# Kernel optimization log

Hardware: AMD Instinct MI355X
Metric: run time of the kernel (lower is better)

The kernel has to match this reference:

```python
import jax, jax.numpy as jnp
import numpy as np

# Model dims (match init_kwargs)
B, S, D = 4, 2048, 1024          # batch, seq, d_model
H, E, DH = 8, 4, 128             # n_heads, n_experts_attn, d_head
K = 2                            # k_attn (routed, n_expert_shared_attn=0)
NEG_INF = jnp.float32(-1e30)


def setup_inputs() -> dict:
    key = jax.random.key(0)
    ks = jax.random.split(key, 9)
    s = np.float32(1.0 / np.sqrt(D))
    return {
        "q_src": jax.random.normal(ks[0], (B, S, D), jnp.float32),
        "k_src": jax.random.normal(ks[1], (B, S, D), jnp.float32),
        "v_src": jax.random.normal(ks[2], (B, S, D), jnp.float32),
        "wq": jax.random.normal(ks[3], (H * DH, D), jnp.float32) * s,
        "wk": jax.random.normal(ks[4], (H * DH, D), jnp.float32) * s,
        "sel_v_w": jax.random.normal(ks[5], (H * E, D), jnp.float32) * s,
        "sel_o_w": jax.random.normal(ks[6], (H * E, D), jnp.float32) * s,
        "v_w": jax.random.normal(ks[7], (H, E, D, DH), jnp.float32) * s,
        "o_w": jax.random.normal(ks[8], (H, E, DH, D), jnp.float32) * np.float32(1.0 / np.sqrt(H * DH)),
        "bias_v": jnp.zeros((E,), jnp.float32),   # load-balancing bias buffer (zeros at init)
        "bias_o": jnp.zeros((E,), jnp.float32),
        # causal boolean mask, True = attend (skip_mask all True -> trimming is identity)
        "attn_mask": jnp.broadcast_to(jnp.tril(jnp.ones((S, S), bool)), (B, S, S)),
        "position_ids": jnp.broadcast_to(jnp.arange(S, dtype=jnp.int32), (B, S)),
        "skip_mask": jnp.ones((B, S), bool),
    }


def _expert_gate(x, w, bias):
    """Sigmoid gating + per-head top-k routed expert selection.
    Returns dense combine weights [b,s,h,E] (sum of sel_val * one_hot) and indices [b,s,h,K]."""
    logits = (x @ w.T).reshape(*x.shape[:-1], H, E)        # [b,s,h,E]
    sel = jax.nn.sigmoid(logits)
    # bias only affects *which* experts are picked (added under no_grad in torch)
    _, idx = jax.lax.top_k(jax.lax.stop_gradient(sel) + bias, K)  # [b,s,h,K]
    sel_val = jnp.take_along_axis(sel, idx, axis=-1)        # [b,s,h,K]
    gate = jnp.sum(jax.nn.one_hot(idx, E, dtype=sel.dtype) * sel_val[..., None], axis=-2)
    return gate, idx


def reference(q_src, k_src, v_src, wq, wk, sel_v_w, sel_o_w, v_w, o_w,
              bias_v, bias_o, attn_mask, position_ids, skip_mask):
    # scale.sqrt() applied to both q and k -> full 1/sqrt(d_head) on scores
    ssq = jnp.float32((1.0 / np.sqrt(DH)) ** 0.5)
    q = ((q_src @ wq.T) * ssq).reshape(B, S, H, DH).transpose(0, 2, 1, 3)  # [b,h,s,dh]
    k = ((k_src @ wk.T) * ssq).reshape(B, S, H, DH).transpose(0, 2, 1, 3)

    v_gate, v_idx = _expert_gate(k_src, sel_v_w, bias_v)    # V experts routed on k_src
    o_gate, o_idx = _expert_gate(q_src, sel_o_w, bias_o)    # O experts routed on q_src

    # expert-mixed V projection (cvmm): all experts then dense combine
    all_v = jnp.einsum('bsm,hemd->bshed', v_src, v_w)       # [b,s,h,E,dh]
    v = jnp.einsum('bshed,bshe->bhsd', all_v, v_gate)       # [b,h,s,dh]

    scores = jnp.einsum('bhqd,bhkd->bhqk', q, k)
    scores = jnp.where(attn_mask[:, None], scores, NEG_INF)
    attn = jax.nn.softmax(scores, axis=-1)
    out = jnp.einsum('bhqk,bhkd->bqhd', attn, v)            # [b,s,h,dh]

    # expert-mixed O projection, summed over heads
    scaled = out[..., None, :] * o_gate[..., None]          # [b,s,h,E,dh]
    res = jnp.einsum('bshed,hedm->bsm', scaled, o_w)        # [b,s,d_model]
    return res, (v_idx, o_idx)
```

## Files before the change

### kernel.cpp

```cpp
#include <hip/hip_runtime.h>
#include <cstdint>
#include <cstddef>

typedef __bf16 bf16;
typedef __bf16 bf16x4 __attribute__((ext_vector_type(4)));
typedef __bf16 bf16x8 __attribute__((ext_vector_type(8)));
typedef float  fx4    __attribute__((ext_vector_type(4)));


__device__ __forceinline__ void async16(const void* g, void* l) {
  __builtin_amdgcn_global_load_lds((const __attribute__((address_space(1))) void*)g,
                                   (__attribute__((address_space(3))) void*)l, 16, 0, 0);
}

#define BARRIER() do { asm volatile("" ::: "memory"); __builtin_amdgcn_s_barrier(); \
                       asm volatile("" ::: "memory"); } while (0)

template <int CTRL>
__device__ __forceinline__ float dppf(float x) {
  return __int_as_float(__builtin_amdgcn_update_dpp(
      0, __float_as_int(x), CTRL, 0xf, 0xf, true));
}

__global__ __launch_bounds__(256) void f32_to_bf16(const float4* __restrict__ src,
                                                   bf16x4* __restrict__ dst, int n4) {
  int i = blockIdx.x * 256 + threadIdx.x;
  if (i < n4) {
    float4 v = src[i];
    bf16x4 o;
    o[0] = (bf16)v.x; o[1] = (bf16)v.y; o[2] = (bf16)v.z; o[3] = (bf16)v.w;
    dst[i] = o;
  }
}

__global__ __launch_bounds__(256) void make_wvt(const float* __restrict__ v_w,
                                                bf16* __restrict__ wvt) {
  __shared__ float tile[64][65];
  const int he = blockIdx.z, k0 = blockIdx.x * 64, dh0 = blockIdx.y * 64;
  const float* in = v_w + (size_t)he * 1024 * 128;
  #pragma unroll
  for (int j = 0; j < 16; j++) {
    int idx = threadIdx.x + j * 256;
    int r = idx >> 6, c = idx & 63;
    tile[r][c] = in[(size_t)(k0 + r) * 128 + dh0 + c];
  }
  __syncthreads();
  const int h = he >> 2, e = he & 3;
  bf16* outp = wvt + ((size_t)(h * 128 + dh0) * 4 + e) * 1024 + k0;
  #pragma unroll
  for (int j = 0; j < 16; j++) {
    int idx = threadIdx.x + j * 256;
    int r = idx >> 6, c = idx & 63;
    outp[(size_t)r * 4096 + c] = (bf16)tile[c][r];
  }
}

__global__ __launch_bounds__(256) void make_wot(const float* __restrict__ o_w,
                                                bf16* __restrict__ wot) {
  __shared__ float tile[64][65];
  const int he = blockIdx.z, d0 = blockIdx.x * 64, dh0 = blockIdx.y * 64;
  const float* in = o_w + (size_t)he * 128 * 1024;
  #pragma unroll
  for (int j = 0; j < 16; j++) {
    int idx = threadIdx.x + j * 256;
    int r = idx >> 6, c = idx & 63;
    tile[r][c] = in[(size_t)(dh0 + r) * 1024 + d0 + c];
  }
  __syncthreads();
  bf16* outp = wot + (size_t)d0 * 4096 + he * 128 + dh0;
  #pragma unroll
  for (int j = 0; j < 16; j++) {
    int idx = threadIdx.x + j * 256;
    int r = idx >> 6, c = idx & 63;
    outp[(size_t)r * 4096 + c] = (bf16)tile[c][r];
  }
}

__global__ __launch_bounds__(256) void gating(const float* __restrict__ q_src,
                                              const float* __restrict__ k_src,
                                              const float* __restrict__ sel_v_w,
                                              const float* __restrict__ sel_o_w,
                                              const float* __restrict__ bias_v,
                                              const float* __restrict__ bias_o,
                                              float* __restrict__ gate_v,
                                              float* __restrict__ gate_o,
                                              float* __restrict__ d_out) {
  const int g = blockIdx.y;
  const int m0 = blockIdx.x * 64;
  const float* x = g ? q_src : k_src;
  const float* w = g ? sel_o_w : sel_v_w;
  const float* bias = g ? bias_o : bias_v;
  float* gate = g ? gate_o : gate_v;
  float* idxo = d_out + 8388608 + g * 131072;

  __shared__ __align__(16) float smem[2 * 12288];

  const int t = threadIdx.x;
  const int hg = t & 7;
  const int tg = t >> 3;

  auto stage = [&](int buf, int k0) {
    float* xs = smem + buf * 12288;
    float* ws = xs + 8192;
    #pragma unroll
    for (int p = 0; p < 8; p++) {
      int of = p * 1024 + t * 4;
      int row = of >> 7, c = (of >> 2) & 31;
      int sc = c ^ ((row >> 1) & 7);
      async16(x + (size_t)(m0 + row) * 1024 + k0 + sc * 4, xs + of);
    }
    #pragma unroll
    for (int p = 0; p < 4; p++) {
      int of = p * 1024 + t * 4;
      int row = of >> 7, c = (of >> 2) & 31;
      int sc = c ^ ((row >> 2) & 7);
      async16(w + (size_t)row * 1024 + k0 + sc * 4, ws + of);
    }
  };

  double acc[2][4] = {};

  stage(0, 0);
  int buf = 0;
  for (int c8 = 0; c8 < 8; c8++) {
    if (c8 < 7) {
      stage(buf ^ 1, (c8 + 1) * 128);
      asm volatile("s_waitcnt vmcnt(12)" ::: "memory");
    } else {
      asm volatile("s_waitcnt vmcnt(0)" ::: "memory");
    }
    BARRIER();
    const float* xs = smem + buf * 12288;
    const float* ws = xs + 8192;
    const int xr0 = tg * 2;
    #pragma unroll 4
    for (int k4 = 0; k4 < 32; k4++) {
      float4 x0 = *(const float4*)(xs + (size_t)xr0 * 128 + (size_t)((k4 ^ (tg & 7)) * 4));
      float4 x1 = *(const float4*)(xs + (size_t)(xr0 + 1) * 128 + (size_t)((k4 ^ (tg & 7)) * 4));
      double x0d[4] = {(double)x0.x, (double)x0.y, (double)x0.z, (double)x0.w};
      double x1d[4] = {(double)x1.x, (double)x1.y, (double)x1.z, (double)x1.w};
      #pragma unroll
      for (int e = 0; e < 4; e++) {
        int wr = hg * 4 + e;
        float4 wv = *(const float4*)(ws + (size_t)wr * 128 + (size_t)((k4 ^ hg) * 4));
        double w0 = (double)wv.x, w1 = (double)wv.y, w2 = (double)wv.z, w3 = (double)wv.w;
        acc[0][e] += x0d[0] * w0 + x0d[1] * w1 + x0d[2] * w2 + x0d[3] * w3;
        acc[1][e] += x1d[0] * w0 + x1d[1] * w1 + x1d[2] * w2 + x1d[3] * w3;
      }
    }
    BARRIER();
    buf ^= 1;
  }

  const float log2e = 1.4426950408889634f;
  float b0 = bias[0], b1 = bias[1], b2 = bias[2], b3 = bias[3];
  #pragma unroll
  for (int tok = 0; tok < 2; tok++) {
    int m = m0 + tg * 2 + tok;
    float sel[4];
    #pragma unroll
    for (int e = 0; e < 4; e++) {
      float lv = (float)acc[tok][e];
      sel[e] = 1.0f / (1.0f + __builtin_amdgcn_exp2f(-lv * log2e));
    }
    float vb[4] = {sel[0] + b0, sel[1] + b1, sel[2] + b2, sel[3] + b3};
    int i0 = 0;
    #pragma unroll
    for (int e = 1; e < 4; e++) if (vb[e] > vb[i0]) i0 = e;
    int i1 = -1; float best = -1e30f;
    #pragma unroll
    for (int e = 0; e < 4; e++) { if (e == i0) continue; if (vb[e] > best) { best = vb[e]; i1 = e; } }
    float4 gv;
    gv.x = (i0 == 0 || i1 == 0) ? sel[0] : 0.f;
    gv.y = (i0 == 1 || i1 == 1) ? sel[1] : 0.f;
    gv.z = (i0 == 2 || i1 == 2) ? sel[2] : 0.f;
    gv.w = (i0 == 3 || i1 == 3) ? sel[3] : 0.f;
    *(float4*)(gate + ((size_t)m * 8 + hg) * 4) = gv;
    idxo[m * 16 + hg * 2 + 0] = (float)i0;
    idxo[m * 16 + hg * 2 + 1] = (float)i1;
  }
}

__global__ __launch_bounds__(256) void expand_o(const bf16* __restrict__ outb,
                                                const float* __restrict__ gate_o,
                                                bf16* __restrict__ Ae) {
  int idx = blockIdx.x * 256 + threadIdx.x;
  int m = idx >> 9;
  int u = idx & 511;
  int he = u >> 4;
  int hh = he >> 2, e = he & 3;
  int dh0 = (u & 15) * 8;
  float gv = gate_o[((size_t)m * 8 + hh) * 4 + e];
  bf16x8 v = *(const bf16x8*)(outb + ((size_t)m * 8 + hh) * 128 + dh0);
  #pragma unroll
  for (int j = 0; j < 8; j++) v[j] = (bf16)((float)v[j] * gv);
  *(bf16x8*)(Ae + (size_t)m * 4096 + u * 8) = v;
}

template <int MODE>
__global__ __launch_bounds__(512) void gemm_moe(const bf16* __restrict__ Abf,
                                                const bf16* __restrict__ BT,
                                                const float* __restrict__ gate,
                                                bf16* __restrict__ Cbf,
                                                float* __restrict__ Cf32,
                                                float scale) {
  constexpr int KDIM = (MODE == 0) ? 1024 : 4096;
  constexpr int ASTRIDE = (MODE == 2) ? 4096 : 1024;
  __shared__ __align__(16) bf16 smem[49152];
  const int t = threadIdx.x;
  const int wave = t >> 6, lane = t & 63;
  const int wr = wave >> 1, wc = wave & 1;
  const int quad = lane >> 4, l16 = lane & 15;
  const int bid = blockIdx.x;
  const int m0 = (bid >> 3) * 256;
  const int n0 = (MODE == 1) ? 0 : (bid & 7) * 128;
  const int h = (MODE == 1) ? (bid & 7) : 0;
  const bf16* BTh = (MODE == 1) ? BT + (size_t)h * 128 * 4096 : BT;

  fx4 acc[4][4] = {};
  fx4 accT[4][4] = {};

  const int srow = t >> 3, sch = t & 7;

  auto stage = [&](int buf, int k0) {
    bf16* As = smem + buf * 16384;
    bf16* Bs = smem + 32768 + buf * 8192;
    #pragma unroll
    for (int p = 0; p < 2; p++) {
      int row = p * 64 + srow;
      int sc = sch ^ (row & 7);
      async16(BTh + (size_t)(n0 + row) * KDIM + k0 + sc * 8,
              Bs + row * 64 + sch * 8);
    }
    int col = (MODE == 1) ? (k0 & 1023) : k0;
    #pragma unroll
    for (int p = 0; p < 4; p++) {
      int row = p * 64 + srow;
      int sc = sch ^ (row & 7);
      async16(Abf + (size_t)(m0 + row) * ASTRIDE + col + sc * 8,
              As + row * 64 + sch * 8);
    }
  };

  stage(0, 0);
  int buf = 0;
  for (int k0 = 0; k0 < KDIM; k0 += 64) {
    if (k0 + 64 < KDIM) {
      stage(buf ^ 1, k0 + 64);
      asm volatile("s_waitcnt vmcnt(6)" ::: "memory");
    } else {
      asm volatile("s_waitcnt vmcnt(0)" ::: "memory");
    }
    BARRIER();
    const bf16* As = smem + buf * 16384;
    const bf16* Bs = smem + 32768 + buf * 8192;
    #pragma unroll
    for (int kk = 0; kk < 64; kk += 32) {
      bf16x8 af[4], bfr[4];
      #pragma unroll
      for (int i = 0; i < 4; i++) {
        int ar = wr * 64 + i * 16 + l16;
        af[i] = *(const bf16x8*)(As + ar * 64 + ((((kk >> 3) + quad) ^ (ar & 7)) * 8));
      }
      #pragma unroll
      for (int i = 0; i < 2; i++) {
        int br = wc * 64 + i * 16 + l16;
        bfr[i] = *(const bf16x8*)(Bs + br * 64 + ((((kk >> 3) + quad) ^ (br & 7)) * 8));
      }
      BARRIER();
      __builtin_amdgcn_s_setprio(1);
      #pragma unroll
      for (int mi = 0; mi < 4; mi++)
        #pragma unroll
        for (int ni = 0; ni < 2; ni++)
          acc[mi][ni] = __builtin_amdgcn_mfma_f32_16x16x32_bf16(af[mi], bfr[ni], acc[mi][ni], 0, 0, 0);
      __builtin_amdgcn_s_setprio(0);
      BARRIER();
      #pragma unroll
      for (int i = 2; i < 4; i++) {
        int br = wc * 64 + i * 16 + l16;
        bfr[i] = *(const bf16x8*)(Bs + br * 64 + ((((kk >> 3) + quad) ^ (br & 7)) * 8));
      }
      BARRIER();
      __builtin_amdgcn_s_setprio(1);
      #pragma unroll
      for (int mi = 0; mi < 4; mi++)
        #pragma unroll
        for (int ni = 2; ni < 4; ni++)
          acc[mi][ni] = __builtin_amdgcn_mfma_f32_16x16x32_bf16(af[mi], bfr[ni], acc[mi][ni], 0, 0, 0);
      __builtin_amdgcn_s_setprio(0);
      BARRIER();
    }
    if constexpr (MODE == 1) {
      if (((k0 + 64) & 1023) == 0) {
        const int e = k0 >> 10;
        #pragma unroll
        for (int mi = 0; mi < 4; mi++)
          #pragma unroll
          for (int r = 0; r < 4; r++) {
            int m = m0 + wr * 64 + mi * 16 + quad * 4 + r;
            float gv = gate[((size_t)m * 8 + h) * 4 + e];
            #pragma unroll
            for (int ni = 0; ni < 4; ni++)
              accT[mi][ni][r] += gv * acc[mi][ni][r];
          }
        #pragma unroll
        for (int mi = 0; mi < 4; mi++)
          #pragma unroll
          for (int ni = 0; ni < 4; ni++)
            #pragma unroll
            for (int j = 0; j < 4; j++) acc[mi][ni][j] = 0.f;
      }
    }
    buf ^= 1;
  }

  if (MODE == 1) {
    #pragma unroll
    for (int mi = 0; mi < 4; mi++)
      #pragma unroll
      for (int ni = 0; ni < 4; ni++) {
        int nl = wc * 64 + ni * 16 + l16;
        int ml = wr * 64 + mi * 16 + quad * 4;
        bf16x4 pk;
        #pragma unroll
        for (int r = 0; r < 4; r++) pk[r] = (bf16)accT[mi][ni][r];
        *(bf16x4*)(smem + nl * 264 + ml) = pk;
      }
    __syncthreads();
    int b = m0 >> 11, s0 = m0 & 2047;
    const int row = t >> 2, seg = t & 3;
    bf16* dst = Cbf + (((size_t)(b * 8 + h) * 128) + row) * 2048 + s0 + seg * 64;
    #pragma unroll
    for (int j = 0; j < 8; j++)
      *(float4*)(dst + j * 8) = *(float4*)(smem + row * 264 + seg * 64 + j * 8);
    return;
  }

  #pragma unroll
  for (int mi = 0; mi < 4; mi++)
    #pragma unroll
    for (int ni = 0; ni < 4; ni++)
      #pragma unroll
      for (int r = 0; r < 4; r++) {
        int m = m0 + wr * 64 + mi * 16 + quad * 4 + r;
        int n = n0 + wc * 64 + ni * 16 + l16;
        float v = acc[mi][ni][r] * scale;
        if (MODE == 0) {
          int b = m >> 11, s = m & 2047, hh = n >> 7, dh = n & 127;
          Cbf[(((size_t)(b * 8 + hh) * 2048 + s) << 7) + dh] = (bf16)v;
        } else {
          Cf32[(size_t)m * 1024 + n] = v;
        }
      }
}

__global__ __launch_bounds__(256) void attn_kernel(const bf16* __restrict__ qb,
                                                   const bf16* __restrict__ kb,
                                                   const bf16* __restrict__ vbT,
                                                   bf16* __restrict__ outb) {
  const int bh = blockIdx.y;
  const int b = bh >> 3, h = bh & 7;
  __shared__ __align__(16) bf16 Ks[2][64 * 128];
  __shared__ __align__(16) bf16 VTs[2][128 * 64];
  __shared__ __align__(16) bf16 Ps[4][16][72];
  const int t = threadIdx.x, wave = t >> 6, lane = t & 63;
  const int quad = lane >> 4, l16 = lane & 15;
  const bf16* qbase  = qb  + (size_t)bh * 2048 * 128;
  const bf16* kbase  = kb  + (size_t)bh * 2048 * 128;
  const bf16* vtbase = vbT + (size_t)bh * 128 * 2048;

  auto stage = [&](int buf, int kt) {
    #pragma unroll
    for (int p = 0; p < 4; p++) {
      int o = p * 4096 + wave * 1024 + lane * 16;
      int kr = o >> 8, kc = o & 255;
      async16((const char*)kbase + (size_t)(kt * 64 + kr) * 256 + (kc ^ ((kr & 7) << 4)),
              (char*)&Ks[buf][0] + o);
    }
    #pragma unroll
    for (int p = 0; p < 4; p++) {
      int o = p * 4096 + wave * 1024 + lane * 16;
      int vr = o >> 7, vc = o & 127;
      async16((const char*)vtbase + (size_t)vr * 4096 + kt * 128 + (vc ^ ((vr & 7) << 4)),
              (char*)&VTs[buf][0] + o);
    }
  };

  #pragma unroll 1
  for (int pass = 0; pass < 2; pass++) {
    const int qt = pass ? blockIdx.x : (31 - blockIdx.x);

    bf16x8 qf[4];
    #pragma unroll
    for (int dk = 0; dk < 4; dk++)
      qf[dk] = *(const bf16x8*)(qbase + (size_t)(qt * 64 + wave * 16 + l16) * 128 + dk * 32 + quad * 8);

    float m_run[4], l_run[4];
    fx4 acc_o[8] = {};
    #pragma unroll
    for (int r = 0; r < 4; r++) { m_run[r] = -1e30f; l_run[r] = 0.f; }

    stage(0, 0);
    int cur = 0;

    for (int kt = 0; kt <= qt; kt++) {
      if (kt < qt) {
        stage(cur ^ 1, kt + 1);
        asm volatile("s_waitcnt vmcnt(8)" ::: "memory");
      } else {
        asm volatile("s_waitcnt vmcnt(0)" ::: "memory");
      }
      __builtin_amdgcn_s_barrier();
      asm volatile("" ::: "memory");

      const char* Ksb  = (const char*)&Ks[cur][0];
      const char* VTsb = (const char*)&VTs[cur][0];

      fx4 accs[4] = {};
      __builtin_amdgcn_s_setprio(1);
      #pragma unroll
      for (int ni = 0; ni < 4; ni++)
        #pragma unroll
        for (int dk = 0; dk < 4; dk++) {
          int r = ni * 16 + l16;
          bf16x8 kf = *(const bf16x8*)(Ksb + r * 256 + ((dk * 64 + quad * 16) ^ ((r & 7) << 4)));
          accs[ni] = __builtin_amdgcn_mfma_f32_16x16x32_bf16(qf[dk], kf, accs[ni], 0, 0, 0);
        }
      __builtin_amdgcn_s_setprio(0);

      if (kt == qt) {
        #pragma unroll
        for (int ni = 0; ni < 4; ni++)
          #pragma unroll
          for (int r = 0; r < 4; r++) {
            int qr = wave * 16 + quad * 4 + r;
            int kc = ni * 16 + l16;
            if (kc > qr) accs[ni][r] = -1e30f;
          }
      }

      #pragma unroll
      for (int r = 0; r < 4; r++) {
        float mx = fmaxf(fmaxf(accs[0][r], accs[1][r]), fmaxf(accs[2][r], accs[3][r]));
        mx = fmaxf(mx, dppf<0x121>(mx));
        mx = fmaxf(mx, dppf<0x122>(mx));
        mx = fmaxf(mx, dppf<0x124>(mx));
        mx = fmaxf(mx, dppf<0x128>(mx));
        float m_new = fmaxf(m_run[r], mx);
        float alpha = __builtin_amdgcn_exp2f(m_run[r] - m_new);
        float rs = 0.f;
        #pragma unroll
        for (int ni = 0; ni < 4; ni++) {
          float p = __builtin_amdgcn_exp2f(accs[ni][r] - m_new);
          accs[ni][r] = p; rs += p;
        }
        rs += dppf<0x121>(rs);
        rs += dppf<0x122>(rs);
        rs += dppf<0x124>(rs);
        rs += dppf<0x128>(rs);
        l_run[r] = l_run[r] * alpha + rs;
        m_run[r] = m_new;
        #pragma unroll
        for (int nj = 0; nj < 8; nj++) acc_o[nj][r] *= alpha;
      }

      #pragma unroll
      for (int ni = 0; ni < 4; ni++)
        #pragma unroll
        for (int r = 0; r < 4; r++)
          Ps[wave][quad * 4 + r][ni * 16 + l16] = (bf16)accs[ni][r];

      __builtin_amdgcn_s_setprio(1);
      #pragma unroll
      for (int step = 0; step < 2; step++) {
        bf16x8 pf = *(const bf16x8*)&Ps[wave][l16][step * 32 + quad * 8];
        #pragma unroll
        for (int nj = 0; nj < 8; nj++) {
          int r = nj * 16 + l16;
          bf16x8 vf = *(const bf16x8*)(VTsb + r * 128 + ((step * 64 + quad * 16) ^ ((r & 7) << 4)));
          acc_o[nj] = __builtin_amdgcn_mfma_f32_16x16x32_bf16(pf, vf, acc_o[nj], 0, 0, 0);
        }
      }
      __builtin_amdgcn_s_setprio(0);

      asm volatile("" ::: "memory");
      __builtin_amdgcn_s_barrier();
      cur ^= 1;
    }

    #pragma unroll
    for (int nj = 0; nj < 8; nj++)
      #pragma unroll
      for (int r = 0; r < 4; r++) {
        int s = qt * 64 + wave * 16 + quad * 4 + r;
        int token = b * 2048 + s;
        float o = acc_o[nj][r] / l_run[r];
        outb[((size_t)token * 8 + h) * 128 + nj * 16 + l16] = (bf16)o;
      }
  }
}

extern "C" void kernel_launch(void* const* d_in, const int* in_sizes, int n_in,
                              void* d_out, int out_size, void* d_ws, size_t ws_size,
                              hipStream_t stream) {
  const float* q_src  = (const float*)d_in[0];
  const float* k_src  = (const float*)d_in[1];
  const float* v_src  = (const float*)d_in[2];
  const float* wq     = (const float*)d_in[3];
  const float* wk     = (const float*)d_in[4];
  const float* sel_v_w = (const float*)d_in[5];
  const float* sel_o_w = (const float*)d_in[6];
  const float* v_w    = (const float*)d_in[7];
  const float* o_w    = (const float*)d_in[8];
  const float* bias_v = (const float*)d_in[9];
  const float* bias_o = (const float*)d_in[10];
  float* out = (float*)d_out;

  char* ws = (char*)d_ws;
  size_t off = 0;
  auto alloc = [&](size_t bytes) { char* p = ws + off; off += (bytes + 255) & ~(size_t)255; return p; };
  bf16* wqb   = (bf16*)alloc((size_t)1024 * 1024 * 2);
  bf16* wkb   = (bf16*)alloc((size_t)1024 * 1024 * 2);
  bf16* wvt   = (bf16*)alloc((size_t)8 * 128 * 4 * 1024 * 2);
  bf16* wot   = (bf16*)alloc((size_t)1024 * 4096 * 2);
  float* gate_v = (float*)alloc((size_t)8192 * 32 * 4);
  float* gate_o = (float*)alloc((size_t)8192 * 32 * 4);
  bf16* qsb   = (bf16*)alloc((size_t)8192 * 1024 * 2);
  bf16* ksb   = (bf16*)alloc((size_t)8192 * 1024 * 2);
  bf16* vsb   = (bf16*)alloc((size_t)8192 * 1024 * 2);
  bf16* qb    = (bf16*)alloc((size_t)8192 * 1024 * 2);
  bf16* kb    = (bf16*)alloc((size_t)8192 * 1024 * 2);
  bf16* vbT   = (bf16*)alloc((size_t)8192 * 1024 * 2);
  bf16* outb  = (bf16*)alloc((size_t)8192 * 1024 * 2);
  bf16* Ae    = qsb;

  f32_to_bf16<<<1024, 256, 0, stream>>>((const float4*)wq, (bf16x4*)wqb, 262144);
  f32_to_bf16<<<1024, 256, 0, stream>>>((const float4*)wk, (bf16x4*)wkb, 262144);
  f32_to_bf16<<<8192, 256, 0, stream>>>((const float4*)q_src, (bf16x4*)qsb, 2097152);
  f32_to_bf16<<<8192, 256, 0, stream>>>((const float4*)k_src, (bf16x4*)ksb, 2097152);
  f32_to_bf16<<<8192, 256, 0, stream>>>((const float4*)v_src, (bf16x4*)vsb, 2097152);
  make_wvt<<<dim3(16, 2, 32), 256, 0, stream>>>(v_w, wvt);
  make_wot<<<dim3(16, 2, 32), 256, 0, stream>>>(o_w, wot);
  gating<<<dim3(128, 2), 256, 0, stream>>>(q_src, k_src, sel_v_w, sel_o_w,
                                           bias_v, bias_o, gate_v, gate_o, out);

  const float ssq = 0.29730177875068026f;
  const float log2e = 1.4426950408889634f;
  gemm_moe<0><<<256, 512, 0, stream>>>(qsb, wqb, nullptr, qb, nullptr, ssq * log2e);
  gemm_moe<0><<<256, 512, 0, stream>>>(ksb, wkb, nullptr, kb, nullptr, ssq);
  gemm_moe<1><<<256, 512, 0, stream>>>(vsb, wvt, gate_v, vbT, nullptr, 1.0f);
  attn_kernel<<<dim3(16, 32), 256, 0, stream>>>(qb, kb, vbT, outb);
  expand_o<<<16384, 256, 0, stream>>>(outb, gate_o, Ae);
  gemm_moe<2><<<256, 512, 0, stream>>>(Ae, wot, nullptr, nullptr, out, 1.0f);
}
```

Before: 597.4 us.

## Merge launches, fuse gate expansion into attention, defer softmax rescale

Merges the five f32->bf16 conversions into one launch, the two weight transposes into one, and the Q and K projection GEMMs into a single 512-block launch. The expand_o pass is folded into the attention epilogue, which writes gate-scaled outputs straight into the expert-expanded buffer. This removes a separate read/write pass over the expanded buffer but adds scattered 2-byte stores from attention. The online softmax skips the rescale of the output accumulator when every row's new max stays within 8 (log2 units) of the running max. Attention blocks are also remapped so neighbouring blocks hit different batch/head pairs.

```diff
diff --git a/kernel.cpp b/kernel.cpp
--- a/kernel.cpp
+++ b/kernel.cpp
@@ -22,57 +22,70 @@
       0, __float_as_int(x), CTRL, 0xf, 0xf, true));
 }
 
-__global__ __launch_bounds__(256) void f32_to_bf16(const float4* __restrict__ src,
-                                                   bf16x4* __restrict__ dst, int n4) {
+__global__ __launch_bounds__(256) void cvt_all(const float4* __restrict__ q,
+                                               const float4* __restrict__ k,
+                                               const float4* __restrict__ v,
+                                               const float4* __restrict__ wq,
+                                               const float4* __restrict__ wk,
+                                               bf16x4* __restrict__ qo, bf16x4* __restrict__ ko,
+                                               bf16x4* __restrict__ vo, bf16x4* __restrict__ wqo,
+                                               bf16x4* __restrict__ wko) {
+  const int y = blockIdx.y;
+  const float4* s; bf16x4* d; int n4;
+  if      (y == 0) { s = q;  d = qo;  n4 = 2097152; }
+  else if (y == 1) { s = k;  d = ko;  n4 = 2097152; }
+  else if (y == 2) { s = v;  d = vo;  n4 = 2097152; }
+  else if (y == 3) { s = wq; d = wqo; n4 = 262144; }
+  else             { s = wk; d = wko; n4 = 262144; }
   int i = blockIdx.x * 256 + threadIdx.x;
   if (i < n4) {
-    float4 v = src[i];
+    float4 t = s[i];
     bf16x4 o;
-    o[0] = (bf16)v.x; o[1] = (bf16)v.y; o[2] = (bf16)v.z; o[3] = (bf16)v.w;
-    dst[i] = o;
-  }
-}
-
-__global__ __launch_bounds__(256) void make_wvt(const float* __restrict__ v_w,
-                                                bf16* __restrict__ wvt) {
+    o[0] = (bf16)t.x; o[1] = (bf16)t.y; o[2] = (bf16)t.z; o[3] = (bf16)t.w;
+    d[i] = o;
+  }
+}
+
+__global__ __launch_bounds__(256) void make_w(const float* __restrict__ v_w,
+                                              const float* __restrict__ o_w,
+                                              bf16* __restrict__ wvt,
+                                              bf16* __restrict__ wot) {
   __shared__ float tile[64][65];
-  const int he = blockIdx.z, k0 = blockIdx.x * 64, dh0 = blockIdx.y * 64;
-  const float* in = v_w + (size_t)he * 1024 * 128;
-  #pragma unroll
-  for (int j = 0; j < 16; j++) {
-    int idx = threadIdx.x + j * 256;
-    int r = idx >> 6, c = idx & 63;
-    tile[r][c] = in[(size_t)(k0 + r) * 128 + dh0 + c];
-  }
-  __syncthreads();
-  const int h = he >> 2, e = he & 3;
-  bf16* outp = wvt + ((size_t)(h * 128 + dh0) * 4 + e) * 1024 + k0;
-  #pragma unroll
-  for (int j = 0; j < 16; j++) {
-    int idx = threadIdx.x + j * 256;
-    int r = idx >> 6, c = idx & 63;
-    outp[(size_t)r * 4096 + c] = (bf16)tile[c][r];
-  }
-}
-
-__global__ __launch_bounds__(256) void make_wot(const float* __restrict__ o_w,
-                                                bf16* __restrict__ wot) {
-  __shared__ float tile[64][65];
-  const int he = blockIdx.z, d0 = blockIdx.x * 64, dh0 = blockIdx.y * 64;
-  const float* in = o_w + (size_t)he * 128 * 1024;
-  #pragma unroll
-  for (int j = 0; j < 16; j++) {
-    int idx = threadIdx.x + j * 256;
-    int r = idx >> 6, c = idx & 63;
-    tile[r][c] = in[(size_t)(dh0 + r) * 1024 + d0 + c];
-  }
-  __syncthreads();
-  bf16* outp = wot + (size_t)d0 * 4096 + he * 128 + dh0;
-  #pragma unroll
-  for (int j = 0; j < 16; j++) {
-    int idx = threadIdx.x + j * 256;
-    int r = idx >> 6, c = idx & 63;
-    outp[(size_t)r * 4096 + c] = (bf16)tile[c][r];
+  if (blockIdx.z < 32) {
+    const int he = blockIdx.z, k0 = blockIdx.x * 64, dh0 = blockIdx.y * 64;
+    const float* in = v_w + (size_t)he * 1024 * 128;
+    #pragma unroll
+    for (int j = 0; j < 16; j++) {
+      int idx = threadIdx.x + j * 256;
+      int r = idx >> 6, c = idx & 63;
+      tile[r][c] = in[(size_t)(k0 + r) * 128 + dh0 + c];
+    }
+    __syncthreads();
+    const int h = he >> 2, e = he & 3;
+    bf16* outp = wvt + ((size_t)(h * 128 + dh0) * 4 + e) * 1024 + k0;
+    #pragma unroll
+    for (int j = 0; j < 16; j++) {
+      int idx = threadIdx.x + j * 256;
+      int r = idx >> 6, c = idx & 63;
+      outp[(size_t)r * 4096 + c] = (bf16)tile[c][r];
+    }
+  } else {
+    const int he = blockIdx.z - 32, d0 = blockIdx.x * 64, dh0 = blockIdx.y * 64;
+    const float* in = o_w + (size_t)he * 128 * 1024;
+    #pragma unroll
+    for (int j = 0; j < 16; j++) {
+      int idx = threadIdx.x + j * 256;
+      int r = idx >> 6, c = idx & 63;
+      tile[r][c] = in[(size_t)(dh0 + r) * 1024 + d0 + c];
+    }
+    __syncthreads();
+    bf16* outp = wot + (size_t)d0 * 4096 + he * 128 + dh0;
+    #pragma unroll
+    for (int j = 0; j < 16; j++) {
+      int idx = threadIdx.x + j * 256;
+      int r = idx >> 6, c = idx & 63;
+      outp[(size_t)r * 4096 + c] = (bf16)tile[c][r];
+    }
   }
 }
 
@@ -181,29 +194,17 @@
   }
 }
 
-__global__ __launch_bounds__(256) void expand_o(const bf16* __restrict__ outb,
-                                                const float* __restrict__ gate_o,
-                                                bf16* __restrict__ Ae) {
-  int idx = blockIdx.x * 256 + threadIdx.x;
-  int m = idx >> 9;
-  int u = idx & 511;
-  int he = u >> 4;
-  int hh = he >> 2, e = he & 3;
-  int dh0 = (u & 15) * 8;
-  float gv = gate_o[((size_t)m * 8 + hh) * 4 + e];
-  bf16x8 v = *(const bf16x8*)(outb + ((size_t)m * 8 + hh) * 128 + dh0);
-  #pragma unroll
-  for (int j = 0; j < 8; j++) v[j] = (bf16)((float)v[j] * gv);
-  *(bf16x8*)(Ae + (size_t)m * 4096 + u * 8) = v;
-}
-
 template <int MODE>
 __global__ __launch_bounds__(512) void gemm_moe(const bf16* __restrict__ Abf,
                                                 const bf16* __restrict__ BT,
                                                 const float* __restrict__ gate,
                                                 bf16* __restrict__ Cbf,
                                                 float* __restrict__ Cf32,
-                                                float scale) {
+                                                float scale,
+                                                const bf16* __restrict__ Abf2,
+                                                const bf16* __restrict__ BT2,
+                                                bf16* __restrict__ Cbf2,
+                                                float scale2) {
   constexpr int KDIM = (MODE == 0) ? 1024 : 4096;
   constexpr int ASTRIDE = (MODE == 2) ? 4096 : 1024;
   __shared__ __align__(16) bf16 smem[49152];
@@ -212,10 +213,16 @@
   const int wr = wave >> 1, wc = wave & 1;
   const int quad = lane >> 4, l16 = lane & 15;
   const int bid = blockIdx.x;
-  const int m0 = (bid >> 3) * 256;
-  const int n0 = (MODE == 1) ? 0 : (bid & 7) * 128;
-  const int h = (MODE == 1) ? (bid & 7) : 0;
-  const bf16* BTh = (MODE == 1) ? BT + (size_t)h * 128 * 4096 : BT;
+  const int sel = (MODE == 0) ? (bid >> 8) : 0;
+  const bf16* A  = sel ? Abf2 : Abf;
+  const bf16* Bt = sel ? BT2  : BT;
+  bf16* Cb       = sel ? Cbf2 : Cbf;
+  const float scl = sel ? scale2 : scale;
+  const int lbid = (MODE == 0) ? (bid & 255) : bid;
+  const int m0 = (lbid >> 3) * 256;
+  const int n0 = (MODE == 1) ? 0 : (lbid & 7) * 128;
+  const int h = (MODE == 1) ? (lbid & 7) : 0;
+  const bf16* BTh = (MODE == 1) ? Bt + (size_t)h * 128 * 4096 : Bt;
 
   fx4 acc[4][4] = {};
   fx4 accT[4][4] = {};
@@ -237,7 +244,7 @@
     for (int p = 0; p < 4; p++) {
       int row = p * 64 + srow;
       int sc = sch ^ (row & 7);
-      async16(Abf + (size_t)(m0 + row) * ASTRIDE + col + sc * 8,
+      async16(A + (size_t)(m0 + row) * ASTRIDE + col + sc * 8,
               As + row * 64 + sch * 8);
     }
   };
@@ -330,7 +337,7 @@
     __syncthreads();
     int b = m0 >> 11, s0 = m0 & 2047;
     const int row = t >> 2, seg = t & 3;
-    bf16* dst = Cbf + (((size_t)(b * 8 + h) * 128) + row) * 2048 + s0 + seg * 64;
+    bf16* dst = Cb + (((size_t)(b * 8 + h) * 128) + row) * 2048 + s0 + seg * 64;
     #pragma unroll
     for (int j = 0; j < 8; j++)
       *(float4*)(dst + j * 8) = *(float4*)(smem + row * 264 + seg * 64 + j * 8);
@@ -345,10 +352,10 @@
       for (int r = 0; r < 4; r++) {
         int m = m0 + wr * 64 + mi * 16 + quad * 4 + r;
         int n = n0 + wc * 64 + ni * 16 + l16;
-        float v = acc[mi][ni][r] * scale;
+        float v = acc[mi][ni][r] * scl;
         if (MODE == 0) {
           int b = m >> 11, s = m & 2047, hh = n >> 7, dh = n & 127;
-          Cbf[(((size_t)(b * 8 + hh) * 2048 + s) << 7) + dh] = (bf16)v;
+          Cb[(((size_t)(b * 8 + hh) * 2048 + s) << 7) + dh] = (bf16)v;
         } else {
           Cf32[(size_t)m * 1024 + n] = v;
         }
@@ -358,8 +365,11 @@
 __global__ __launch_bounds__(256) void attn_kernel(const bf16* __restrict__ qb,
                                                    const bf16* __restrict__ kb,
                                                    const bf16* __restrict__ vbT,
-                                                   bf16* __restrict__ outb) {
-  const int bh = blockIdx.y;
+                                                   const float* __restrict__ gate_o,
+                                                   bf16* __restrict__ Ae) {
+  const int linear = blockIdx.y * 16 + blockIdx.x;
+  const int bh = (linear & 7) * 4 + ((linear >> 3) & 3);
+  const int px = linear >> 5;
   const int b = bh >> 3, h = bh & 7;
   __shared__ __align__(16) bf16 Ks[2][64 * 128];
   __shared__ __align__(16) bf16 VTs[2][128 * 64];
@@ -389,7 +399,7 @@
 
   #pragma unroll 1
   for (int pass = 0; pass < 2; pass++) {
-    const int qt = pass ? blockIdx.x : (31 - blockIdx.x);
+    const int qt = pass ? px : (31 - px);
 
     bf16x8 qf[4];
     #pragma unroll
@@ -440,6 +450,7 @@
           }
       }
 
+      float mxv[4];
       #pragma unroll
       for (int r = 0; r < 4; r++) {
         float mx = fmaxf(fmaxf(accs[0][r], accs[1][r]), fmaxf(accs[2][r], accs[3][r]));
@@ -447,22 +458,45 @@
         mx = fmaxf(mx, dppf<0x122>(mx));
         mx = fmaxf(mx, dppf<0x124>(mx));
         mx = fmaxf(mx, dppf<0x128>(mx));
-        float m_new = fmaxf(m_run[r], mx);
-        float alpha = __builtin_amdgcn_exp2f(m_run[r] - m_new);
-        float rs = 0.f;
-        #pragma unroll
-        for (int ni = 0; ni < 4; ni++) {
-          float p = __builtin_amdgcn_exp2f(accs[ni][r] - m_new);
-          accs[ni][r] = p; rs += p;
+        mxv[r] = mx;
+      }
+      bool defer = (mxv[0] <= m_run[0] + 8.f) && (mxv[1] <= m_run[1] + 8.f) &&
+                   (mxv[2] <= m_run[2] + 8.f) && (mxv[3] <= m_run[3] + 8.f);
+      if (__all(defer)) {
+        #pragma unroll
+        for (int r = 0; r < 4; r++) {
+          float rs = 0.f;
+          #pragma unroll
+          for (int ni = 0; ni < 4; ni++) {
+            float p = __builtin_amdgcn_exp2f(accs[ni][r] - m_run[r]);
+            accs[ni][r] = p; rs += p;
+          }
+          rs += dppf<0x121>(rs);
+          rs += dppf<0x122>(rs);
+          rs += dppf<0x124>(rs);
+          rs += dppf<0x128>(rs);
+          l_run[r] += rs;
         }
-        rs += dppf<0x121>(rs);
-        rs += dppf<0x122>(rs);
-        rs += dppf<0x124>(rs);
-        rs += dppf<0x128>(rs);
-        l_run[r] = l_run[r] * alpha + rs;
-        m_run[r] = m_new;
-        #pragma unroll
-        for (int nj = 0; nj < 8; nj++) acc_o[nj][r] *= alpha;
+      } else {
+        #pragma unroll
+        for (int r = 0; r < 4; r++) {
+          float m_new = fmaxf(m_run[r], mxv[r]);
+          float alpha = __builtin_amdgcn_exp2f(m_run[r] - m_new);
+          float rs = 0.f;
+          #pragma unroll
+          for (int ni = 0; ni < 4; ni++) {
+            float p = __builtin_amdgcn_exp2f(accs[ni][r] - m_new);
+            accs[ni][r] = p; rs += p;
+          }
+          rs += dppf<0x121>(rs);
+          rs += dppf<0x122>(rs);
+          rs += dppf<0x124>(rs);
+          rs += dppf<0x128>(rs);
+          l_run[r] = l_run[r] * alpha + rs;
+          m_run[r] = m_new;
+          #pragma unroll
+          for (int nj = 0; nj < 8; nj++) acc_o[nj][r] *= alpha;
+        }
       }
 
       #pragma unroll
@@ -490,14 +524,21 @@
     }
 
     #pragma unroll
-    for (int nj = 0; nj < 8; nj++)
-      #pragma unroll
-      for (int r = 0; r < 4; r++) {
-        int s = qt * 64 + wave * 16 + quad * 4 + r;
-        int token = b * 2048 + s;
-        float o = acc_o[nj][r] / l_run[r];
-        outb[((size_t)token * 8 + h) * 128 + nj * 16 + l16] = (bf16)o;
-      }
+    for (int r = 0; r < 4; r++) {
+      int s = qt * 64 + wave * 16 + quad * 4 + r;
+      int token = b * 2048 + s;
+      float4 g4 = *(const float4*)(gate_o + ((size_t)token * 8 + h) * 4);
+      float inv = 1.0f / l_run[r];
+      #pragma unroll
+      for (int nj = 0; nj < 8; nj++) {
+        float o = acc_o[nj][r] * inv;
+        bf16* dst = Ae + (size_t)token * 4096 + (h * 4) * 128 + nj * 16 + l16;
+        dst[0]   = (bf16)(o * g4.x);
+        dst[128] = (bf16)(o * g4.y);
+        dst[256] = (bf16)(o * g4.z);
+        dst[384] = (bf16)(o * g4.w);
+      }
+    }
   }
 }
 
@@ -529,28 +570,27 @@
   bf16* qsb   = (bf16*)alloc((size_t)8192 * 1024 * 2);
   bf16* ksb   = (bf16*)alloc((size_t)8192 * 1024 * 2);
   bf16* vsb   = (bf16*)alloc((size_t)8192 * 1024 * 2);
+  (void)alloc((size_t)8192 * 1024 * 2);
+  bf16* Ae    = qsb;
   bf16* qb    = (bf16*)alloc((size_t)8192 * 1024 * 2);
   bf16* kb    = (bf16*)alloc((size_t)8192 * 1024 * 2);
   bf16* vbT   = (bf16*)alloc((size_t)8192 * 1024 * 2);
-  bf16* outb  = (bf16*)alloc((size_t)8192 * 1024 * 2);
-  bf16* Ae    = qsb;
-
-  f32_to_bf16<<<1024, 256, 0, stream>>>((const float4*)wq, (bf16x4*)wqb, 262144);
-  f32_to_bf16<<<1024, 256, 0, stream>>>((const float4*)wk, (bf16x4*)wkb, 262144);
-  f32_to_bf16<<<8192, 256, 0, stream>>>((const float4*)q_src, (bf16x4*)qsb, 2097152);
-  f32_to_bf16<<<8192, 256, 0, stream>>>((const float4*)k_src, (bf16x4*)ksb, 2097152);
-  f32_to_bf16<<<8192, 256, 0, stream>>>((const float4*)v_src, (bf16x4*)vsb, 2097152);
-  make_wvt<<<dim3(16, 2, 32), 256, 0, stream>>>(v_w, wvt);
-  make_wot<<<dim3(16, 2, 32), 256, 0, stream>>>(o_w, wot);
+
+  cvt_all<<<dim3(8192, 5), 256, 0, stream>>>((const float4*)q_src, (const float4*)k_src,
+                                             (const float4*)v_src, (const float4*)wq,
+                                             (const float4*)wk, (bf16x4*)qsb, (bf16x4*)ksb,
+                                             (bf16x4*)vsb, (bf16x4*)wqb, (bf16x4*)wkb);
+  make_w<<<dim3(16, 2, 64), 256, 0, stream>>>(v_w, o_w, wvt, wot);
   gating<<<dim3(128, 2), 256, 0, stream>>>(q_src, k_src, sel_v_w, sel_o_w,
                                            bias_v, bias_o, gate_v, gate_o, out);
 
   const float ssq = 0.29730177875068026f;
   const float log2e = 1.4426950408889634f;
-  gemm_moe<0><<<256, 512, 0, stream>>>(qsb, wqb, nullptr, qb, nullptr, ssq * log2e);
-  gemm_moe<0><<<256, 512, 0, stream>>>(ksb, wkb, nullptr, kb, nullptr, ssq);
-  gemm_moe<1><<<256, 512, 0, stream>>>(vsb, wvt, gate_v, vbT, nullptr, 1.0f);
-  attn_kernel<<<dim3(16, 32), 256, 0, stream>>>(qb, kb, vbT, outb);
-  expand_o<<<16384, 256, 0, stream>>>(outb, gate_o, Ae);
-  gemm_moe<2><<<256, 512, 0, stream>>>(Ae, wot, nullptr, nullptr, out, 1.0f);
-}
+  gemm_moe<0><<<512, 512, 0, stream>>>(qsb, wqb, nullptr, qb, nullptr, ssq * log2e,
+                                       ksb, wkb, kb, ssq);
+  gemm_moe<1><<<256, 512, 0, stream>>>(vsb, wvt, gate_v, vbT, nullptr, 1.0f,
+                                       nullptr, nullptr, nullptr, 0.f);
+  attn_kernel<<<dim3(16, 32), 256, 0, stream>>>(qb, kb, vbT, gate_o, Ae);
+  gemm_moe<2><<<256, 512, 0, stream>>>(Ae, wot, nullptr, nullptr, out, 1.0f,
+                                       nullptr, nullptr, nullptr, 0.f);
+}
```

Measured after the change: 570.6 us. -4.5%, faster.
